# Kernel optimization log

Hardware: AMD Instinct MI355X
Metric: run time of the kernel (lower is better)

The kernel has to match this reference:

```python
import jax, jax.numpy as jnp
import numpy as np

# ---- static config (mirrors init_kwargs) ----
B, E, L, CH = 2, 512, 128, 256      # batch, encoding_channels, latent_dim, channels
W = 512                              # window_size
STEP = W // 2                        # 256
NC = W // 2 + 1                      # 257 rfft coeffs
RS = 32768                           # resonance_samples
NF = RS // STEP                      # 128 frames
BASE_RES = 0.5
RES_FACTOR = (1.0 - BASE_RES) * 0.999


def setup_inputs() -> dict:
    key = jax.random.key(0)
    ks = jax.random.split(key, 8)
    return {
        "latents": jax.random.normal(ks[0], (B, E, L), jnp.float32),
        "phase0_u": jax.random.uniform(ks[1], (B, 1, E, NC), jnp.float32),
        "noise_u": jax.random.uniform(ks[2], (B, NF, E, NC), jnp.float32),
        "Win": jax.random.normal(ks[3], (3, L, CH), jnp.float32) / np.float32(np.sqrt(L)),
        "b_in": jnp.zeros((3, CH), jnp.float32),
        "Wh": jax.random.normal(ks[4], (3, 2, CH, CH), jnp.float32) / np.float32(np.sqrt(CH)),
        "b_h": jnp.zeros((3, 2, CH), jnp.float32),
        "Wout": jax.random.normal(ks[5], (3, CH, NC), jnp.float32) / np.float32(np.sqrt(CH)),
        "b_out": jnp.zeros((3, NC), jnp.float32),
    }


def _ln(x):
    # LayerNorm over last dim, no learned affine
    m = jnp.mean(x, -1, keepdims=True)
    v = jnp.var(x, -1, keepdims=True)
    return (x - m) * jax.lax.rsqrt(v + 1e-5)


def _stacks(latents, Win, b_in, Wh, b_h, Wout, b_out):
    # three LinearOutputStacks (to_initial / to_resonance / to_phase_dither)
    h = jnp.einsum('bel,slc->sbec', latents, Win) + b_in[:, None, None, :]
    for k in range(2):
        h = _ln(jax.nn.leaky_relu(h, 0.2))
        h = jnp.einsum('sbec,scd->sbed', h, Wh[:, k]) + b_h[:, k, None, None, :]
    h = _ln(jax.nn.leaky_relu(h, 0.2))
    return jnp.einsum('sbec,scn->sben', h, Wout) + b_out[:, None, None, :]


def reference(latents, phase0_u, noise_u, Win, b_in, Wh, b_h, Wout, b_out):
    out3 = _stacks(latents, Win, b_in, Wh, b_h, Wout, b_out)  # [3,B,E,NC]
    initial, res_pre, dith_pre = out3[0], out3[1], out3[2]
    res = BASE_RES + jax.nn.sigmoid(res_pre) * RES_FACTOR      # (0.5, ~1.0)
    dither = jax.nn.sigmoid(dith_pre)

    t = jnp.arange(NF, dtype=jnp.float32)[None, :, None, None]  # [1,NF,1,1]
    # sequential decay  mag_t = initial * res^t  (fused cumprod)
    mags = initial[:, None] * jnp.exp(t * jnp.log(res)[:, None])  # [B,NF,E,NC]

    gd = jnp.linspace(0.0, np.pi, NC).astype(jnp.float32)        # group delay
    phase0 = (phase0_u * 2.0 - 1.0) * np.float32(np.pi)
    noise = (noise_u * 2.0 - 1.0) * np.float32(np.pi)
    noise = noise.at[:, 0].set(0.0)  # first frame has no dither step
    # sequential phase accumulation as cumsum
    phases = phase0 + t * gd + jnp.cumsum(dither[:, None] * noise, axis=1)

    frames = jax.lax.complex(mags * jnp.cos(phases), mags * jnp.sin(phases))
    windowed = jnp.fft.irfft(frames, n=W, axis=-1, norm='ortho')  # [B,NF,E,W]
    windowed = jnp.transpose(windowed, (0, 2, 1, 3))              # [B,E,NF,W]

    # overlap-add with Hann window, hop = STEP = W//2
    win = (0.5 - 0.5 * jnp.cos(2.0 * np.pi * jnp.arange(W) / W)).astype(jnp.float32)
    xw = windowed * win
    a = xw[..., :STEP].reshape(B, E, NF * STEP)
    b = xw[..., STEP:].reshape(B, E, NF * STEP)
    out = jnp.zeros((B, E, (NF + 1) * STEP), jnp.float32)
    out = out.at[..., :NF * STEP].add(a)
    out = out.at[..., STEP:].add(b)
    return out[..., :RS]  # [B,E,RS]
```

## Files before the change

### kernel.cpp

```cpp
#include <hip/hip_runtime.h>
#include <hip/hip_bf16.h>

#define PI_F 3.14159265358979323846f

typedef short  bf16x8 __attribute__((ext_vector_type(8)));
typedef unsigned short u16x8 __attribute__((ext_vector_type(8)));
typedef float  f32x4  __attribute__((ext_vector_type(4)));

#define OUT3_OFF  0
#define TPACK_OFF 3158016
#define WPACK_OFF (3158016 + 65536)

static __device__ __forceinline__ unsigned short f2bf(float x) {
    unsigned int u = __float_as_uint(x);
    unsigned int r = (u + 0x7fffu + ((u >> 16) & 1u)) >> 16;
    return (unsigned short)r;
}

static __device__ __forceinline__ unsigned int pk_bf16(float a, float b) {
    unsigned int r;
    asm("v_cvt_pk_bf16_f32 %0, %1, %2" : "=v"(r) : "v"(a), "v"(b));
    return r;
}

static __device__ __forceinline__ float sigm(float x) {
    return 1.f / (1.f + expf(-x));
}

static __device__ __forceinline__ float bf_lo(unsigned int u) {
    return __uint_as_float(u << 16);
}
static __device__ __forceinline__ float bf_hi(unsigned int u) {
    return __uint_as_float(u & 0xffff0000u);
}

__global__ __launch_bounds__(256) void wpack(
    const float* __restrict__ Win, const float* __restrict__ Wh,
    const float* __restrict__ Wout, unsigned short* __restrict__ wp)
{
    int g = blockIdx.x * 256 + threadIdx.x;
    int t = g >> 6, l = g & 63;
    int s = t / 448, lt = t % 448;
    int layer, base;
    if (lt < 64)       { layer = 0; base = 0;   }
    else if (lt < 192) { layer = 1; base = 64;  }
    else if (lt < 320) { layer = 2; base = 192; }
    else               { layer = 3; base = 320; }
    int local = lt - base, ks = local >> 4, nt = local & 15;

    u16x8 hv, lv;
    #pragma unroll
    for (int j = 0; j < 8; ++j) {
        int k = ks*32 + ((l >> 4) << 3) + j;
        int n = nt*16 + (l & 15);
        float w;
        if (layer == 0)      w = Win[(size_t)s*32768 + k*256 + n];
        else if (layer == 1) w = Wh[((size_t)s*2 + 0)*65536 + k*256 + n];
        else if (layer == 2) w = Wh[((size_t)s*2 + 1)*65536 + k*256 + n];
        else                 w = Wout[(size_t)s*65792 + k*257 + n];
        unsigned int ph = pk_bf16(w, 0.f);
        float fh = bf_lo(ph);
        hv[j] = (unsigned short)(ph & 0xffffu);
        lv[j] = (unsigned short)(pk_bf16(w - fh, 0.f) & 0xffffu);
    }
    *(u16x8*)(wp + (size_t)(t*2    )*512 + l*8) = hv;
    *(u16x8*)(wp + (size_t)(t*2 + 1)*512 + l*8) = lv;
}

__global__ __launch_bounds__(512) void mlp_mfma(
    const float* __restrict__ latents,
    const float* __restrict__ b_in, const float* __restrict__ b_h,
    const float* __restrict__ b_out, const float* __restrict__ Wout,
    const unsigned short* __restrict__ wp,
    float* __restrict__ out3)
{
    __shared__ float xs[64*260];
    __shared__ unsigned int xh[64*132];
    __shared__ unsigned int xl[64*132];
    __shared__ float mrow[64], rrow[64];

    const int tid  = threadIdx.x;
    const int s    = blockIdx.y;
    const int row0 = blockIdx.x * 64;
    const int l  = tid & 63;
    const int wv = tid >> 6;
    const int m0 = l & 15;
    const int ac = l >> 4;

    const int4* Wp4 = (const int4*)wp;
    const int4* xh4 = (const int4*)xh;
    const int4* xl4 = (const int4*)xl;

    #pragma unroll
    for (int i = 0; i < 8; ++i) {
        int idx = tid + i*512;
        int r = idx >> 6, kp = idx & 63;
        const float* lp = latents + (size_t)(row0 + r)*128 + 2*kp;
        float x0 = lp[0], x1 = lp[1];
        unsigned int u = pk_bf16(x0, x1);
        xh[r*132 + kp] = u;
        xl[r*132 + kp] = pk_bf16(x0 - bf_lo(u), x1 - bf_hi(u));
    }
    __syncthreads();

    for (int L = 0; L < 4; ++L) {
        const int kt    = (L == 0) ? 4 : 8;
        const int tbase = s*448 + ((L == 0) ? 0 : (L == 1) ? 64 : (L == 2) ? 192 : 320);

        f32x4 acc[4][2];
        #pragma unroll
        for (int mt = 0; mt < 4; ++mt) {
            acc[mt][0] = (f32x4){0.f, 0.f, 0.f, 0.f};
            acc[mt][1] = (f32x4){0.f, 0.f, 0.f, 0.f};
        }

        for (int ks = 0; ks < kt; ++ks) {
            const int t0 = tbase + ks*16 + wv*2;
            int4 bh0 = Wp4[(size_t)(t0*2    )*64 + l];
            int4 bl0 = Wp4[(size_t)(t0*2 + 1)*64 + l];
            int4 bh1 = Wp4[(size_t)(t0*2 + 2)*64 + l];
            int4 bl1 = Wp4[(size_t)(t0*2 + 3)*64 + l];
            bf16x8 BH0 = *(bf16x8*)&bh0, BL0 = *(bf16x8*)&bl0;
            bf16x8 BH1 = *(bf16x8*)&bh1, BL1 = *(bf16x8*)&bl1;
            #pragma unroll
            for (int mt = 0; mt < 4; ++mt) {
                int4 ah = xh4[(m0 + 16*mt)*33 + ks*4 + ac];
                int4 al = xl4[(m0 + 16*mt)*33 + ks*4 + ac];
                bf16x8 AH = *(bf16x8*)&ah, AL = *(bf16x8*)&al;
                acc[mt][0] = __builtin_amdgcn_mfma_f32_16x16x32_bf16(AH, BH0, acc[mt][0], 0, 0, 0);
                acc[mt][0] = __builtin_amdgcn_mfma_f32_16x16x32_bf16(AH, BL0, acc[mt][0], 0, 0, 0);
                acc[mt][0] = __builtin_amdgcn_mfma_f32_16x16x32_bf16(AL, BH0, acc[mt][0], 0, 0, 0);
                acc[mt][1] = __builtin_amdgcn_mfma_f32_16x16x32_bf16(AH, BH1, acc[mt][1], 0, 0, 0);
                acc[mt][1] = __builtin_amdgcn_mfma_f32_16x16x32_bf16(AH, BL1, acc[mt][1], 0, 0, 0);
                acc[mt][1] = __builtin_amdgcn_mfma_f32_16x16x32_bf16(AL, BH1, acc[mt][1], 0, 0, 0);
            }
        }

        if (L < 3) {
            const float* bias = (L == 0) ? (b_in + s*256) : (b_h + (s*2 + (L-1))*256);
            const float bb0 = bias[wv*32 + m0];
            const float bb1 = bias[wv*32 + 16 + m0];
            #pragma unroll
            for (int mt = 0; mt < 4; ++mt)
                #pragma unroll
                for (int r = 0; r < 4; ++r) {
                    int row = mt*16 + ac*4 + r;
                    float v0 = acc[mt][0][r] + bb0;
                    float v1 = acc[mt][1][r] + bb1;
                    v0 = (v0 >= 0.f) ? v0 : 0.2f*v0;
                    v1 = (v1 >= 0.f) ? v1 : 0.2f*v1;
                    xs[row*260 + wv*32 + m0]      = v0;
                    xs[row*260 + wv*32 + 16 + m0] = v1;
                }
            __syncthreads();

            #pragma unroll
            for (int i = 0; i < 8; ++i) {
                int row = wv*8 + i;
                float s1 = 0.f, s2 = 0.f;
                #pragma unroll
                for (int j = 0; j < 4; ++j) {
                    float v = xs[row*260 + l + 64*j];
                    s1 += v; s2 += v*v;
                }
                #pragma unroll
                for (int o = 32; o > 0; o >>= 1) {
                    s1 += __shfl_xor(s1, o, 64);
                    s2 += __shfl_xor(s2, o, 64);
                }
                if (l == 0) {
                    float m   = s1 * (1.f/256.f);
                    float var = s2 * (1.f/256.f) - m*m;
                    mrow[row] = m;
                    rrow[row] = rsqrtf(var + 1e-5f);
                }
            }
            __syncthreads();

            #pragma unroll
            for (int i = 0; i < 16; ++i) {
                int idx = tid + i*512;
                int r = idx >> 7, kp = idx & 127;
                float mm = mrow[r], rr = rrow[r];
                float u = (xs[r*260 + 2*kp    ] - mm) * rr;
                float v = (xs[r*260 + 2*kp + 1] - mm) * rr;
                unsigned int uh = pk_bf16(u, v);
                xh[r*132 + kp] = uh;
                xl[r*132 + kp] = pk_bf16(u - bf_lo(uh), v - bf_hi(uh));
            }
            __syncthreads();
        } else {
            const float* bo = b_out + s*257;
            #pragma unroll
            for (int mt = 0; mt < 4; ++mt)
                #pragma unroll
                for (int r = 0; r < 4; ++r) {
                    int row = mt*16 + ac*4 + r;
                    float* op = out3 + ((size_t)s*1024 + row0 + row)*257;
                    op[wv*32 + m0]      = acc[mt][0][r] + bo[wv*32 + m0];
                    op[wv*32 + 16 + m0] = acc[mt][1][r] + bo[wv*32 + 16 + m0];
                }
            {
                int r  = tid >> 3;
                int c8 = tid & 7;
                float mm = mrow[r], rr = rrow[r];
                float p = 0.f;
                const float* w2 = Wout + (size_t)s*65792 + 256;
                #pragma unroll
                for (int j = 0; j < 32; ++j) {
                    int cc = c8*32 + j;
                    p = fmaf((xs[r*260 + cc] - mm) * rr, w2[(size_t)cc*257], p);
                }
                p += __shfl_xor(p, 1, 64);
                p += __shfl_xor(p, 2, 64);
                p += __shfl_xor(p, 4, 64);
                if (c8 == 0)
                    out3[((size_t)s*1024 + row0 + r)*257 + 256] = p + b_out[s*257 + 256];
            }
        }
    }
}

__global__ __launch_bounds__(256) void tpack_init(unsigned short* __restrict__ tp)
{
    int g = blockIdx.x * 256 + threadIdx.x;
    int tile = g >> 6, l = g & 63;
    int ks = tile >> 3;
    int wv = tile & 7;
    int wg = wv >> 1, p = wv & 1;
    u16x8 v;
    #pragma unroll
    for (int j = 0; j < 8; ++j) {
        int k2 = ks*32 + ((l >> 4) << 3) + j;
        int kap = (k2 >> 1) + 1;
        int w  = wg*32 + 2*(l & 15) + p;
        int m  = (kap * w) & 511;
        float ang = (float)m * (PI_F / 256.f);
        float sn, cn; sincosf(ang, &sn, &cn);
        v[j] = f2bf((k2 & 1) ? sn : cn);
    }
    *(u16x8*)(tp + (size_t)g * 8) = v;
}

__global__ __launch_bounds__(512, 4) void synth_row(
    const float* __restrict__ out3,
    const float* __restrict__ phase0_u,
    const float* __restrict__ noise_u,
    const unsigned short* __restrict__ tpack,
    float* __restrict__ out)
{
    __shared__ __align__(16) unsigned int lds_u[16896];
    __shared__ float a0s[64];
    __shared__ float a256s[64];
    __shared__ float pbuf[8][260];
    __shared__ float xs128[64];
    __shared__ float xs384[64];

    unsigned int* abtP = lds_u;
    unsigned int* abtQ = lds_u + 64*132;
    float*        xbf  = (float*)lds_u;

    const int tid = threadIdx.x;
    const int row = blockIdx.x;
    const int b   = row >> 9;
    const int e   = row & 511;

    const float inv = 0.04419417382415922f;

    float pr = 0.f, dith_ = 0.f, gdd = 0.f;
    if (tid <= 256) {
        float dpre = out3[((size_t)2*1024 + row)*257 + tid];
        dith_ = sigm(dpre);
        float gd = (float)tid * (1.f/512.f);
        gdd = gd - 0.5f*dith_;
        pr  = phase0_u[(size_t)row*257 + tid] - 0.5f;
    }
    float m2 = 0.f, res2_ = 0.f;
    if (tid == 256) {
        float i2 = out3[((size_t)0*1024 + row)*257 + 256];
        float r2 = out3[((size_t)1*1024 + row)*257 + 256];
        res2_ = 0.5f + 0.4995f * sigm(r2);
        m2    = inv * i2;
    }

    const int kc = tid & 255;
    const int j0 = (tid >> 8) * 4;
    float m_base, rp1, rp2, rp3, res8;
    float bsgn = -1.f;
    unsigned int* tgt = abtP;
    {
        float ini  = out3[((size_t)0*1024 + row)*257 + kc];
        float rpre = out3[((size_t)1*1024 + row)*257 + kc];
        float res  = 0.5f + 0.4995f * sigm(rpre);
        float cs   = (kc == 0 ? 1.f : 2.f) * inv;
        rp1 = res;
        rp2 = res * res;
        rp3 = rp2 * res;
        float res4 = rp2 * rp2;
        res8 = res4 * res4;
        m_base = cs * ini;
        if (j0 == 4) m_base *= res4;
        if (kc >= 129)     { tgt = abtQ + (255 - kc); bsgn = 1.f; }
        else if (kc >= 1)  { tgt = abtP + (kc - 1); }
    }

    const float* nrow = noise_u + ((size_t)b*128*512 + e)*257;
    const size_t nstride = (size_t)512*257;

    float h1 = 0.f, h2 = 0.f;
    {
        float c0 = __builtin_amdgcn_cosf((float)tid * (1.f/512.f));
        h1 = 0.5f - 0.5f*c0;
        h2 = 0.5f + 0.5f*c0;
    }
    const float sgn = (tid & 1) ? -1.f : 1.f;
    float tail = 0.f;

    const int l  = tid & 63;
    const int wv = tid >> 6;
    const int m0 = l & 15;
    const int ac = l >> 4;
    const int wsrc = (wv >> 1)*32 + 2*m0 + (wv & 1);
    const int c1 = wsrc;
    const int c2 = wsrc + 256;
    const int c3 = 256 - wsrc;
    const int c4 = 512 - wsrc;
    const bool c4ok = (wsrc != 0);
    const int4* abtP4 = (const int4*)abtP;
    const int4* abtQ4 = (const int4*)abtQ;
    const int4* abtR4 = (wv & 1) ? abtQ4 : abtP4;
    const int4* Tp    = (const int4*)tpack;
    const unsigned int S   = 0x80008000u;
    const unsigned int B31 = 0x80000000u;

    for (int sweep = 0; sweep < 2; ++sweep) {
        const int F0 = sweep * 64;

        for (int g = 0; g < 8; ++g) {
            if (tid <= 256) {
                float nzb[8];
                #pragma unroll
                for (int j = 0; j < 8; ++j) {
                    int t = F0 + g*8 + j;
                    nzb[j] = (t >= 1) ? __builtin_nontemporal_load(
                                            &nrow[(size_t)t*nstride + tid]) : 0.5f;
                }
                #pragma unroll
                for (int j = 0; j < 8; ++j) {
                    int t = F0 + g*8 + j;
                    if (t >= 1) pr += fmaf(dith_, nzb[j], gdd);
                    pbuf[j][tid] = pr;
                    if (tid == 256) {
                        if (t >= 1) m2 *= res2_;
                        float fr = pr - floorf(pr);
                        a256s[g*8 + j] = m2 * __builtin_amdgcn_cosf(fr);
                    }
                }
            } else if (g == 0 && tid >= 448) {
                abtQ[(tid - 448)*132 + 127] = 0;
            }
            __syncthreads();

            {
                const int fb = g*8 + j0;
                float mv[4];
                mv[0] = m_base;
                mv[1] = m_base * rp1;
                mv[2] = m_base * rp2;
                mv[3] = m_base * rp3;
                #pragma unroll
                for (int q = 0; q < 4; ++q) {
                    float p  = pbuf[j0 + q][kc];
                    float fr = p - floorf(p);
                    float sn = __builtin_amdgcn_sinf(fr);
                    float cn = __builtin_amdgcn_cosf(fr);
                    float a  = mv[q] * cn;
                    if (kc == 0) {
                        a0s[fb + q] = a;
                    } else {
                        float bv = bsgn * mv[q] * sn;
                        tgt[(fb + q)*132] = pk_bf16(a, bv);
                    }
                }
                m_base *= res8;
            }
            __syncthreads();
        }

        {
            #pragma unroll
            for (int i = 0; i < 16; ++i) {
                int idx = tid + i*512;
                int f  = idx >> 7, ki = idx & 127;
                int o  = f*132 + ki;
                unsigned int up = abtP[o];
                unsigned int uq = abtQ[o];
                float aP = bf_lo(up), bP = bf_hi(up);
                float aQ = bf_lo(uq), bQ = bf_hi(uq);
                abtP[o] = pk_bf16(aP + aQ, bP + bQ);
                abtQ[o] = pk_bf16(aP - aQ, bP - bQ);
            }
        }
        __syncthreads();

        f32x4 acc1[4], acc2[4], acc3[4], acc4[4];
        #pragma unroll
        for (int mt = 0; mt < 4; ++mt) {
            acc1[mt] = (f32x4){0.f, 0.f, 0.f, 0.f};
            acc2[mt] = (f32x4){0.f, 0.f, 0.f, 0.f};
            acc3[mt] = (f32x4){0.f, 0.f, 0.f, 0.f};
            acc4[mt] = (f32x4){0.f, 0.f, 0.f, 0.f};
        }
        {
            const int r0g = m0*33 + ac;
            for (int ks = 0; ks < 8; ++ks) {
                int4 bi = Tp[(size_t)((ks*8 + wv) << 6) + l];
                bf16x8 B = *(bf16x8*)&bi;
                #pragma unroll
                for (int mt = 0; mt < 4; ++mt) {
                    int4 t = abtR4[r0g + mt*528 + ks*4];
                    acc1[mt] = __builtin_amdgcn_mfma_f32_16x16x32_bf16(*(bf16x8*)&t, B, acc1[mt], 0, 0, 0);
                    t.x ^= S;   t.z ^= S;
                    acc2[mt] = __builtin_amdgcn_mfma_f32_16x16x32_bf16(*(bf16x8*)&t, B, acc2[mt], 0, 0, 0);
                    t.x ^= B31; t.y ^= B31; t.z ^= B31; t.w ^= B31;
                    acc3[mt] = __builtin_amdgcn_mfma_f32_16x16x32_bf16(*(bf16x8*)&t, B, acc3[mt], 0, 0, 0);
                    t.x ^= S;   t.z ^= S;
                    acc4[mt] = __builtin_amdgcn_mfma_f32_16x16x32_bf16(*(bf16x8*)&t, B, acc4[mt], 0, 0, 0);
                }
            }
        }

        {
            const int f8 = tid >> 3;
            const int i8 = tid & 7;
            float s128 = 0.f, s384 = 0.f;
            #pragma unroll
            for (int q = 0; q < 16; ++q) {
                int ki = i8*16 + q;
                unsigned int ue = abtP[f8*132 + ki];
                if ((q + 1) & 1) {
                    float sg = ((q + 1) & 2) ? -1.f : 1.f;
                    float bsum = bf_hi(ue);
                    s128 += sg * bsum;
                    s384 -= sg * bsum;
                } else {
                    float sg = ((q + 1) & 2) ? -1.f : 1.f;
                    float asum = bf_lo(ue);
                    s128 += sg * asum;
                    s384 += sg * asum;
                }
            }
            #pragma unroll
            for (int o = 1; o < 8; o <<= 1) {
                s128 += __shfl_xor(s128, o, 64);
                s384 += __shfl_xor(s384, o, 64);
            }
            if (i8 == 0) { xs128[f8] = s128; xs384[f8] = s384; }
        }
        __syncthreads();

        #pragma unroll
        for (int h = 0; h < 2; ++h) {
            #pragma unroll
            for (int mt2 = 0; mt2 < 2; ++mt2) {
                int mtg = 2*h + mt2;
                #pragma unroll
                for (int r = 0; r < 4; ++r) {
                    int f_loc = mt2*16 + ac*4 + r;
                    float* xr = &xbf[f_loc*516];
                    xr[c1] = acc1[mtg][r];
                    xr[c2] = acc2[mtg][r];
                    xr[c3] = acc3[mtg][r];
                    if (c4ok) xr[c4] = acc4[mtg][r];
                }
            }
            if (tid < 32) {
                xbf[tid*516 + 128] = xs128[h*32 + tid];
                xbf[tid*516 + 384] = xs384[h*32 + tid];
            }
            __syncthreads();
            if (tid < 256) {
                float* orow = out + (size_t)row*32768 + (size_t)(F0 + h*32)*256 + tid;
                #pragma unroll
                for (int f = 0; f < 32; ++f) {
                    int hf = h*32 + f;
                    float s  = a0s[hf] + sgn * a256s[hf];
                    float x1 = xbf[f*516 + tid] + s;
                    float x2 = xbf[f*516 + tid + 256] + s;
                    float v  = fmaf(x1, h1, tail);
                    tail = x2 * h2;
                    __builtin_nontemporal_store(v, &orow[f*256]);
                }
            }
            __syncthreads();
        }
    }
}


extern "C" void kernel_launch(void* const* d_in, const int* in_sizes, int n_in,
                              void* d_out, int out_size, void* d_ws, size_t ws_size,
                              hipStream_t stream)
{
    const float* latents  = (const float*)d_in[0];
    const float* phase0_u = (const float*)d_in[1];
    const float* noise_u  = (const float*)d_in[2];
    const float* Win      = (const float*)d_in[3];
    const float* b_in     = (const float*)d_in[4];
    const float* Wh       = (const float*)d_in[5];
    const float* b_h      = (const float*)d_in[6];
    const float* Wout     = (const float*)d_in[7];
    const float* b_out    = (const float*)d_in[8];

    unsigned char* ws = (unsigned char*)d_ws;
    float*          out3  = (float*)(ws + OUT3_OFF);
    unsigned short* tpack = (unsigned short*)(ws + TPACK_OFF);
    unsigned short* wp    = (unsigned short*)(ws + WPACK_OFF);
    float*          out   = (float*)d_out;

    wpack<<<336, 256, 0, stream>>>(Win, Wh, Wout, wp);
    dim3 gM(16, 3);
    mlp_mfma<<<gM, 512, 0, stream>>>(latents, b_in, b_h, b_out, Wout, wp, out3);
    tpack_init<<<16, 256, 0, stream>>>(tpack);
    synth_row<<<1024, 512, 0, stream>>>(out3, phase0_u, noise_u, tpack, out);
}
```

Before: 166.0 us.

## Shrink MLP row tiles and synth frame sweeps to raise occupancy

The MLP kernel now processes 16 rows per block instead of 64, launching 64x3 blocks instead of 16x3, so more CUs get work. The synthesis kernel splits its 128 frames into four sweeps of 32 instead of two of 64. This halves LDS use and accumulator registers, and the launch bound rises to 6 blocks per CU. The cost is more reloading of weight and twiddle tiles per block, plus more barrier iterations.

Measured after the change: 232.1 us. 39.9% more time.

```diff
diff --git a/kernel.cpp b/kernel.cpp
--- a/kernel.cpp
+++ b/kernel.cpp
@@ -74,14 +74,14 @@
     const unsigned short* __restrict__ wp,
     float* __restrict__ out3)
 {
-    __shared__ float xs[64*260];
-    __shared__ unsigned int xh[64*132];
-    __shared__ unsigned int xl[64*132];
-    __shared__ float mrow[64], rrow[64];
+    __shared__ float xs[16*260];
+    __shared__ unsigned int xh[16*132];
+    __shared__ unsigned int xl[16*132];
+    __shared__ float mrow[16], rrow[16];
 
     const int tid  = threadIdx.x;
     const int s    = blockIdx.y;
-    const int row0 = blockIdx.x * 64;
+    const int row0 = blockIdx.x * 16;
     const int l  = tid & 63;
     const int wv = tid >> 6;
     const int m0 = l & 15;
@@ -92,7 +92,7 @@
     const int4* xl4 = (const int4*)xl;
 
     #pragma unroll
-    for (int i = 0; i < 8; ++i) {
+    for (int i = 0; i < 2; ++i) {
         int idx = tid + i*512;
         int r = idx >> 6, kp = idx & 63;
         const float* lp = latents + (size_t)(row0 + r)*128 + 2*kp;
@@ -107,12 +107,9 @@
         const int kt    = (L == 0) ? 4 : 8;
         const int tbase = s*448 + ((L == 0) ? 0 : (L == 1) ? 64 : (L == 2) ? 192 : 320);
 
-        f32x4 acc[4][2];
-        #pragma unroll
-        for (int mt = 0; mt < 4; ++mt) {
-            acc[mt][0] = (f32x4){0.f, 0.f, 0.f, 0.f};
-            acc[mt][1] = (f32x4){0.f, 0.f, 0.f, 0.f};
-        }
+        f32x4 acc[2];
+        acc[0] = (f32x4){0.f, 0.f, 0.f, 0.f};
+        acc[1] = (f32x4){0.f, 0.f, 0.f, 0.f};
 
         for (int ks = 0; ks < kt; ++ks) {
             const int t0 = tbase + ks*16 + wv*2;
@@ -122,18 +119,15 @@
             int4 bl1 = Wp4[(size_t)(t0*2 + 3)*64 + l];
             bf16x8 BH0 = *(bf16x8*)&bh0, BL0 = *(bf16x8*)&bl0;
             bf16x8 BH1 = *(bf16x8*)&bh1, BL1 = *(bf16x8*)&bl1;
-            #pragma unroll
-            for (int mt = 0; mt < 4; ++mt) {
-                int4 ah = xh4[(m0 + 16*mt)*33 + ks*4 + ac];
-                int4 al = xl4[(m0 + 16*mt)*33 + ks*4 + ac];
-                bf16x8 AH = *(bf16x8*)&ah, AL = *(bf16x8*)&al;
-                acc[mt][0] = __builtin_amdgcn_mfma_f32_16x16x32_bf16(AH, BH0, acc[mt][0], 0, 0, 0);
-                acc[mt][0] = __builtin_amdgcn_mfma_f32_16x16x32_bf16(AH, BL0, acc[mt][0], 0, 0, 0);
-                acc[mt][0] = __builtin_amdgcn_mfma_f32_16x16x32_bf16(AL, BH0, acc[mt][0], 0, 0, 0);
-                acc[mt][1] = __builtin_amdgcn_mfma_f32_16x16x32_bf16(AH, BH1, acc[mt][1], 0, 0, 0);
-                acc[mt][1] = __builtin_amdgcn_mfma_f32_16x16x32_bf16(AH, BL1, acc[mt][1], 0, 0, 0);
-                acc[mt][1] = __builtin_amdgcn_mfma_f32_16x16x32_bf16(AL, BH1, acc[mt][1], 0, 0, 0);
-            }
+            int4 ah = xh4[m0*33 + ks*4 + ac];
+            int4 al = xl4[m0*33 + ks*4 + ac];
+            bf16x8 AH = *(bf16x8*)&ah, AL = *(bf16x8*)&al;
+            acc[0] = __builtin_amdgcn_mfma_f32_16x16x32_bf16(AH, BH0, acc[0], 0, 0, 0);
+            acc[0] = __builtin_amdgcn_mfma_f32_16x16x32_bf16(AH, BL0, acc[0], 0, 0, 0);
+            acc[0] = __builtin_amdgcn_mfma_f32_16x16x32_bf16(AL, BH0, acc[0], 0, 0, 0);
+            acc[1] = __builtin_amdgcn_mfma_f32_16x16x32_bf16(AH, BH1, acc[1], 0, 0, 0);
+            acc[1] = __builtin_amdgcn_mfma_f32_16x16x32_bf16(AH, BL1, acc[1], 0, 0, 0);
+            acc[1] = __builtin_amdgcn_mfma_f32_16x16x32_bf16(AL, BH1, acc[1], 0, 0, 0);
         }
 
         if (L < 3) {
@@ -141,22 +135,20 @@
             const float bb0 = bias[wv*32 + m0];
             const float bb1 = bias[wv*32 + 16 + m0];
             #pragma unroll
-            for (int mt = 0; mt < 4; ++mt)
-                #pragma unroll
-                for (int r = 0; r < 4; ++r) {
-                    int row = mt*16 + ac*4 + r;
-                    float v0 = acc[mt][0][r] + bb0;
-                    float v1 = acc[mt][1][r] + bb1;
-                    v0 = (v0 >= 0.f) ? v0 : 0.2f*v0;
-                    v1 = (v1 >= 0.f) ? v1 : 0.2f*v1;
-                    xs[row*260 + wv*32 + m0]      = v0;
-                    xs[row*260 + wv*32 + 16 + m0] = v1;
-                }
-            __syncthreads();
-
-            #pragma unroll
-            for (int i = 0; i < 8; ++i) {
-                int row = wv*8 + i;
+            for (int r = 0; r < 4; ++r) {
+                int row = ac*4 + r;
+                float v0 = acc[0][r] + bb0;
+                float v1 = acc[1][r] + bb1;
+                v0 = (v0 >= 0.f) ? v0 : 0.2f*v0;
+                v1 = (v1 >= 0.f) ? v1 : 0.2f*v1;
+                xs[row*260 + wv*32 + m0]      = v0;
+                xs[row*260 + wv*32 + 16 + m0] = v1;
+            }
+            __syncthreads();
+
+            #pragma unroll
+            for (int i = 0; i < 2; ++i) {
+                int row = wv*2 + i;
                 float s1 = 0.f, s2 = 0.f;
                 #pragma unroll
                 for (int j = 0; j < 4; ++j) {
@@ -178,7 +170,7 @@
             __syncthreads();
 
             #pragma unroll
-            for (int i = 0; i < 16; ++i) {
+            for (int i = 0; i < 4; ++i) {
                 int idx = tid + i*512;
                 int r = idx >> 7, kp = idx & 127;
                 float mm = mrow[r], rr = rrow[r];
@@ -192,29 +184,29 @@
         } else {
             const float* bo = b_out + s*257;
             #pragma unroll
-            for (int mt = 0; mt < 4; ++mt)
-                #pragma unroll
-                for (int r = 0; r < 4; ++r) {
-                    int row = mt*16 + ac*4 + r;
-                    float* op = out3 + ((size_t)s*1024 + row0 + row)*257;
-                    op[wv*32 + m0]      = acc[mt][0][r] + bo[wv*32 + m0];
-                    op[wv*32 + 16 + m0] = acc[mt][1][r] + bo[wv*32 + 16 + m0];
-                }
+            for (int r = 0; r < 4; ++r) {
+                int row = ac*4 + r;
+                float* op = out3 + ((size_t)s*1024 + row0 + row)*257;
+                op[wv*32 + m0]      = acc[0][r] + bo[wv*32 + m0];
+                op[wv*32 + 16 + m0] = acc[1][r] + bo[wv*32 + 16 + m0];
+            }
             {
-                int r  = tid >> 3;
-                int c8 = tid & 7;
+                int r   = tid >> 5;
+                int c32 = tid & 31;
                 float mm = mrow[r], rr = rrow[r];
                 float p = 0.f;
                 const float* w2 = Wout + (size_t)s*65792 + 256;
                 #pragma unroll
-                for (int j = 0; j < 32; ++j) {
-                    int cc = c8*32 + j;
+                for (int j = 0; j < 8; ++j) {
+                    int cc = c32*8 + j;
                     p = fmaf((xs[r*260 + cc] - mm) * rr, w2[(size_t)cc*257], p);
                 }
                 p += __shfl_xor(p, 1, 64);
                 p += __shfl_xor(p, 2, 64);
                 p += __shfl_xor(p, 4, 64);
-                if (c8 == 0)
+                p += __shfl_xor(p, 8, 64);
+                p += __shfl_xor(p, 16, 64);
+                if (c32 == 0)
                     out3[((size_t)s*1024 + row0 + r)*257 + 256] = p + b_out[s*257 + 256];
             }
         }
@@ -242,22 +234,22 @@
     *(u16x8*)(tp + (size_t)g * 8) = v;
 }
 
-__global__ __launch_bounds__(512, 4) void synth_row(
+__global__ __launch_bounds__(512, 6) void synth_row(
     const float* __restrict__ out3,
     const float* __restrict__ phase0_u,
     const float* __restrict__ noise_u,
     const unsigned short* __restrict__ tpack,
     float* __restrict__ out)
 {
-    __shared__ __align__(16) unsigned int lds_u[16896];
-    __shared__ float a0s[64];
-    __shared__ float a256s[64];
+    __shared__ __align__(16) unsigned int lds_u[8448];
+    __shared__ float a0s[32];
+    __shared__ float a256s[32];
     __shared__ float pbuf[8][260];
-    __shared__ float xs128[64];
-    __shared__ float xs384[64];
+    __shared__ float xs128[32];
+    __shared__ float xs384[32];
 
     unsigned int* abtP = lds_u;
-    unsigned int* abtQ = lds_u + 64*132;
+    unsigned int* abtQ = lds_u + 32*132;
     float*        xbf  = (float*)lds_u;
 
     const int tid = threadIdx.x;
@@ -333,10 +325,10 @@
     const unsigned int S   = 0x80008000u;
     const unsigned int B31 = 0x80000000u;
 
-    for (int sweep = 0; sweep < 2; ++sweep) {
-        const int F0 = sweep * 64;
-
-        for (int g = 0; g < 8; ++g) {
+    for (int sweep = 0; sweep < 4; ++sweep) {
+        const int F0 = sweep * 32;
+
+        for (int g = 0; g < 4; ++g) {
             if (tid <= 256) {
                 float nzb[8];
                 #pragma unroll
@@ -356,8 +348,8 @@
                         a256s[g*8 + j] = m2 * __builtin_amdgcn_cosf(fr);
                     }
                 }
-            } else if (g == 0 && tid >= 448) {
-                abtQ[(tid - 448)*132 + 127] = 0;
+            } else if (g == 0 && tid >= 480) {
+                abtQ[(tid - 480)*132 + 127] = 0;
             }
             __syncthreads();
 
@@ -389,7 +381,7 @@
 
         {
             #pragma unroll
-            for (int i = 0; i < 16; ++i) {
+            for (int i = 0; i < 8; ++i) {
                 int idx = tid + i*512;
                 int f  = idx >> 7, ki = idx & 127;
                 int o  = f*132 + ki;
@@ -403,9 +395,9 @@
         }
         __syncthreads();
 
-        f32x4 acc1[4], acc2[4], acc3[4], acc4[4];
+        f32x4 acc1[2], acc2[2], acc3[2], acc4[2];
         #pragma unroll
-        for (int mt = 0; mt < 4; ++mt) {
+        for (int mt = 0; mt < 2; ++mt) {
             acc1[mt] = (f32x4){0.f, 0.f, 0.f, 0.f};
             acc2[mt] = (f32x4){0.f, 0.f, 0.f, 0.f};
             acc3[mt] = (f32x4){0.f, 0.f, 0.f, 0.f};
@@ -417,7 +409,7 @@
                 int4 bi = Tp[(size_t)((ks*8 + wv) << 6) + l];
                 bf16x8 B = *(bf16x8*)&bi;
                 #pragma unroll
-                for (int mt = 0; mt < 4; ++mt) {
+                for (int mt = 0; mt < 2; ++mt) {
                     int4 t = abtR4[r0g + mt*528 + ks*4];
                     acc1[mt] = __builtin_amdgcn_mfma_f32_16x16x32_bf16(*(bf16x8*)&t, B, acc1[mt], 0, 0, 0);
                     t.x ^= S;   t.z ^= S;
@@ -430,7 +422,7 @@
             }
         }
 
-        {
+        if (tid < 256) {
             const int f8 = tid >> 3;
             const int i8 = tid & 7;
             float s128 = 0.f, s384 = 0.f;
@@ -462,28 +454,24 @@
         #pragma unroll
         for (int h = 0; h < 2; ++h) {
             #pragma unroll
-            for (int mt2 = 0; mt2 < 2; ++mt2) {
-                int mtg = 2*h + mt2;
-                #pragma unroll
-                for (int r = 0; r < 4; ++r) {
-                    int f_loc = mt2*16 + ac*4 + r;
-                    float* xr = &xbf[f_loc*516];
-                    xr[c1] = acc1[mtg][r];
-                    xr[c2] = acc2[mtg][r];
-                    xr[c3] = acc3[mtg][r];
-                    if (c4ok) xr[c4] = acc4[mtg][r];
-                }
-            }
-            if (tid < 32) {
-                xbf[tid*516 + 128] = xs128[h*32 + tid];
-                xbf[tid*516 + 384] = xs384[h*32 + tid];
+            for (int r = 0; r < 4; ++r) {
+                int f_loc = ac*4 + r;
+                float* xr = &xbf[f_loc*516];
+                xr[c1] = acc1[h][r];
+                xr[c2] = acc2[h][r];
+                xr[c3] = acc3[h][r];
+                if (c4ok) xr[c4] = acc4[h][r];
+            }
+            if (tid < 16) {
+                xbf[tid*516 + 128] = xs128[h*16 + tid];
+                xbf[tid*516 + 384] = xs384[h*16 + tid];
             }
             __syncthreads();
             if (tid < 256) {
-                float* orow = out + (size_t)row*32768 + (size_t)(F0 + h*32)*256 + tid;
-                #pragma unroll
-                for (int f = 0; f < 32; ++f) {
-                    int hf = h*32 + f;
+                float* orow = out + (size_t)row*32768 + (size_t)(F0 + h*16)*256 + tid;
+                #pragma unroll
+                for (int f = 0; f < 16; ++f) {
+                    int hf = h*16 + f;
                     float s  = a0s[hf] + sgn * a256s[hf];
                     float x1 = xbf[f*516 + tid] + s;
                     float x2 = xbf[f*516 + tid + 256] + s;
@@ -519,7 +507,7 @@
     float*          out   = (float*)d_out;
 
     wpack<<<336, 256, 0, stream>>>(Win, Wh, Wout, wp);
-    dim3 gM(16, 3);
+    dim3 gM(64, 3);
     mlp_mfma<<<gM, 512, 0, stream>>>(latents, b_in, b_h, b_out, Wout, wp, out3);
     tpack_init<<<16, 256, 0, stream>>>(tpack);
     synth_row<<<1024, 512, 0, stream>>>(out3, phase0_u, noise_u, tpack, out);
```
